# Performance work log

Measured on AMD Instinct MI355X. Metric: run time of the kernel, lower is better.

The kernel has to match this reference:

```python
import jax, jax.numpy as jnp
import numpy as np

T, D = 4096, 1024
S = 32768
DIST_DIM = 20
BINS = jnp.array([1, 2, 3, 4, 8, 16, 32, 64], dtype=jnp.int64)


def setup_inputs() -> dict:
    key = jax.random.key(0)
    ks = jax.random.split(key, 16)
    scale = 1.0 / np.sqrt(D)
    inp = {
        "embeds": jax.random.normal(ks[0], (T, D), dtype=jnp.float32),
        "states": jax.random.normal(ks[1], (T, D), dtype=jnp.float32),
        # MHA (1 head) projection params, torch Linear convention: x @ W.T + b
        "Wq": jax.random.normal(ks[2], (D, D), dtype=jnp.float32) * scale,
        "bq": jnp.zeros((D,), dtype=jnp.float32),
        "Wk": jax.random.normal(ks[3], (D, D), dtype=jnp.float32) * scale,
        "bk": jnp.zeros((D,), dtype=jnp.float32),
        "Wv": jax.random.normal(ks[4], (D, D), dtype=jnp.float32) * scale,
        "bv": jnp.zeros((D,), dtype=jnp.float32),
        "Wo": jax.random.normal(ks[5], (D, D), dtype=jnp.float32) * scale,
        "bo": jnp.zeros((D,), dtype=jnp.float32),
        # distance embedding table: len(bins)+1 = 9 rows
        "dist_embed": jax.random.normal(ks[6], (9, DIST_DIM), dtype=jnp.float32),
        "span_starts": jax.random.randint(ks[7], (S,), 0, T - 30, dtype=jnp.int64),
        "span_lengths": jax.random.randint(ks[8], (S,), 0, 30, dtype=jnp.int64),
    }
    return inp


def reference(embeds, states, Wq, bq, Wk, bk, Wv, bv, Wo, bo, dist_embed,
              span_starts, span_lengths):
    d = states.shape[1]
    # Single-head attention: query=states, key=states, value=embeds (seq len T, batch 1)
    q = states @ Wq.T + bq                      # [T, D]
    k = states @ Wk.T + bk                      # [T, D]
    v = embeds @ Wv.T + bv                      # [T, D]
    scores = (q @ k.T) / jnp.sqrt(jnp.asarray(d, q.dtype))   # [T, T]
    attn = jax.nn.softmax(scores, axis=-1)
    attn_embeds = (attn @ v) @ Wo.T + bo        # [T, D]

    ends = span_starts + span_lengths           # inclusive end, width 1..30
    # ragged per-span segment sum over [start, end] via prefix sums
    cs = jnp.concatenate([jnp.zeros((1, d), attn_embeds.dtype),
                          jnp.cumsum(attn_embeds, axis=0)], axis=0)  # [T+1, D]
    span_sum = cs[ends + 1] - cs[span_starts]   # [S, D]

    span_start_end = jnp.concatenate([states[span_starts], states[ends]], axis=1)  # [S, 2D]

    lengths = span_lengths + 1                  # len(span) = end - start + 1
    bin_idx = jnp.sum(lengths[:, None] > BINS[None, :], axis=-1)  # [S] in [0, 8]
    len_embed = dist_embed[bin_idx]             # [S, DIST_DIM] (dropout omitted: eval mode)

    return jnp.concatenate([span_sum, span_start_end, len_embed], axis=1)  # [S, 3D+20]
```

## Files before the change

### kernel.cpp

```cpp
#include <hip/hip_runtime.h>
#include <hip/hip_bf16.h>


typedef __attribute__((ext_vector_type(8))) short bf16x8;
typedef __attribute__((ext_vector_type(4))) short bf16x4;
typedef __attribute__((ext_vector_type(4))) float f32x4;

#define T_DIM 4096
#define D_DIM 1024
#define S_NUM 32768

#define GLOBAL_LOAD_LDS16(gptr, ldsptr)                                        \
  __builtin_amdgcn_global_load_lds(                                            \
      (const __attribute__((address_space(1))) void*)(gptr),                   \
      (__attribute__((address_space(3))) void*)(ldsptr), 16, 0, 0)

__global__ __launch_bounds__(256) void cast2_bf16(const float* __restrict__ a,
                                                  const float* __restrict__ b,
                                                  __hip_bfloat16* __restrict__ oa,
                                                  __hip_bfloat16* __restrict__ ob) {
  const float* s = blockIdx.z ? b : a;
  __hip_bfloat16* d = blockIdx.z ? ob : oa;
  int i = blockIdx.x * 256 + threadIdx.x;
  float2 v = ((const float2*)s)[i];
  __hip_bfloat162 o;
  o.x = __float2bfloat16(v.x);
  o.y = __float2bfloat16(v.y);
  ((__hip_bfloat162*)d)[i] = o;
}

__global__ __launch_bounds__(256) void cast3_bf16(const float* __restrict__ a,
                                                  const float* __restrict__ b,
                                                  const float* __restrict__ c,
                                                  __hip_bfloat16* __restrict__ oa,
                                                  __hip_bfloat16* __restrict__ ob,
                                                  __hip_bfloat16* __restrict__ oc) {
  const int z = blockIdx.z;
  const float* s = z == 0 ? a : z == 1 ? b : c;
  __hip_bfloat16* d = z == 0 ? oa : z == 1 ? ob : oc;
  int i = blockIdx.x * 256 + threadIdx.x;
  float2 v = ((const float2*)s)[i];
  __hip_bfloat162 o;
  o.x = __float2bfloat16(v.x);
  o.y = __float2bfloat16(v.y);
  ((__hip_bfloat162*)d)[i] = o;
}

__global__ __launch_bounds__(256) void transpose_cast_bf16(const float* __restrict__ in,
                                                           __hip_bfloat16* __restrict__ out) {
  __shared__ float tile[64][65];
  const int bx = blockIdx.x * 64;
  const int by = blockIdx.y * 64;
  const int t = threadIdx.x;
  const int r = t >> 4;
  const int c4 = (t & 15) * 4;
#pragma unroll
  for (int p = 0; p < 4; p++) {
    const float4 v = *(const float4*)&in[(size_t)(by + p * 16 + r) * D_DIM + bx + c4];
    tile[p * 16 + r][c4] = v.x;
    tile[p * 16 + r][c4 + 1] = v.y;
    tile[p * 16 + r][c4 + 2] = v.z;
    tile[p * 16 + r][c4 + 3] = v.w;
  }
  __syncthreads();
#pragma unroll
  for (int p = 0; p < 4; p++) {
    const int orow = p * 16 + r;
    bf16x4 o4;
#pragma unroll
    for (int q = 0; q < 4; q++) {
      __hip_bfloat16 h = __float2bfloat16(tile[c4 + q][orow]);
      o4[q] = *reinterpret_cast<short*>(&h);
    }
    *reinterpret_cast<bf16x4*>(&out[(size_t)(bx + orow) * D_DIM + by + c4]) = o4;
  }
}

__global__ __launch_bounds__(256) void zero_f32(float* __restrict__ p, int n) {
  int i = blockIdx.x * 256 + threadIdx.x;
  if (i < n) p[i] = 0.0f;
}

__global__ __launch_bounds__(256) void bias_fuse(const float* __restrict__ Wo,
                                                 const float* __restrict__ bv,
                                                 const float* __restrict__ bo,
                                                 float* __restrict__ bvo) {
  const int wave = threadIdx.x >> 6, lane = threadIdx.x & 63;
  const int row = blockIdx.x * 4 + wave;
  float s = 0.0f;
  for (int k = lane; k < D_DIM; k += 64) s += Wo[(size_t)row * D_DIM + k] * bv[k];
#pragma unroll
  for (int off = 32; off; off >>= 1) s += __shfl_xor(s, off);
  if (lane == 0) bvo[row] = s + bo[row];
}

__device__ __forceinline__ void gemm_core_128(const __hip_bfloat16* __restrict__ A,
                                              const __hip_bfloat16* __restrict__ B,
                                              int K, int bm, int bn,
                                              __hip_bfloat16* As,
                                              __hip_bfloat16* Bs,
                                              f32x4 acc[4][4]) {
  const int tid = threadIdx.x;
  const int wave = tid >> 6, lane = tid & 63;
  const int srow = lane >> 2, scol = (lane & 3) * 8;
  const __hip_bfloat16* Ag0 = A + (size_t)(bm + wave * 16 + srow) * K + scol;
  const __hip_bfloat16* Ag1 = Ag0 + (size_t)64 * K;
  const __hip_bfloat16* Bg0 = B + (size_t)(bn + wave * 16 + srow) * K + scol;
  const __hip_bfloat16* Bg1 = Bg0 + (size_t)64 * K;
  const int c0 = wave * 512, c1 = (4 + wave) * 512;
  const int wtr = (wave >> 1) * 64, wtc = (wave & 1) * 64;
  const int lr = lane & 15, lk = (lane >> 4) * 8;

  GLOBAL_LOAD_LDS16(Ag0, As + c0);
  GLOBAL_LOAD_LDS16(Ag1, As + c1);
  GLOBAL_LOAD_LDS16(Bg0, Bs + c0);
  GLOBAL_LOAD_LDS16(Bg1, Bs + c1);

  int cur = 0;
  for (int k0 = 0; k0 < K; k0 += 32) {
    __syncthreads();
    const int nxt = cur ^ 1;
    if (k0 + 32 < K) {
      const int kn = k0 + 32;
      GLOBAL_LOAD_LDS16(Ag0 + kn, As + nxt * 4096 + c0);
      GLOBAL_LOAD_LDS16(Ag1 + kn, As + nxt * 4096 + c1);
      GLOBAL_LOAD_LDS16(Bg0 + kn, Bs + nxt * 4096 + c0);
      GLOBAL_LOAD_LDS16(Bg1 + kn, Bs + nxt * 4096 + c1);
    }
    const __hip_bfloat16* a = As + cur * 4096;
    const __hip_bfloat16* b = Bs + cur * 4096;
    bf16x8 af[4], bfr[4];
#pragma unroll
    for (int i = 0; i < 4; i++)
      af[i] = *(const bf16x8*)&a[(wtr + i * 16 + lr) * 32 + lk];
#pragma unroll
    for (int j = 0; j < 4; j++)
      bfr[j] = *(const bf16x8*)&b[(wtc + j * 16 + lr) * 32 + lk];
#pragma unroll
    for (int i = 0; i < 4; i++)
#pragma unroll
      for (int j = 0; j < 4; j++)
        acc[i][j] = __builtin_amdgcn_mfma_f32_16x16x32_bf16(af[i], bfr[j], acc[i][j], 0, 0, 0);
    cur = nxt;
  }
}


__global__ __launch_bounds__(256) void wvo_gemm(const __hip_bfloat16* __restrict__ Wo_bf,
                                                const __hip_bfloat16* __restrict__ WvT_bf,
                                                __hip_bfloat16* __restrict__ Wvo_bf) {
  __shared__ __hip_bfloat16 As[2 * 128 * 32];
  __shared__ __hip_bfloat16 Bs[2 * 128 * 32];
  const int bm = blockIdx.y * 128, bn = blockIdx.x * 128;
  const int wave = threadIdx.x >> 6, lane = threadIdx.x & 63;
  const int wtr = (wave >> 1) * 64, wtc = (wave & 1) * 64;
  const int lr = lane & 15;
  f32x4 acc[4][4] = {};
  gemm_core_128(Wo_bf, WvT_bf, D_DIM, bm, bn, As, Bs, acc);
#pragma unroll
  for (int j = 0; j < 4; j++) {
    const int col = bn + wtc + j * 16 + lr;
#pragma unroll
    for (int i = 0; i < 4; i++)
#pragma unroll
      for (int r = 0; r < 4; r++) {
        const int row = bm + wtr + i * 16 + (lane >> 4) * 4 + r;
        Wvo_bf[(size_t)row * D_DIM + col] = __float2bfloat16(acc[i][j][r]);
      }
  }
}

__global__ __launch_bounds__(256) void qkv_gemm(const __hip_bfloat16* __restrict__ states_bf,
                                                const __hip_bfloat16* __restrict__ embeds_bf,
                                                const __hip_bfloat16* __restrict__ Wq,
                                                const __hip_bfloat16* __restrict__ Wk,
                                                const __hip_bfloat16* __restrict__ Wvo,
                                                const float* __restrict__ bq,
                                                const float* __restrict__ bk,
                                                __hip_bfloat16* __restrict__ q,
                                                __hip_bfloat16* __restrict__ k,
                                                __hip_bfloat16* __restrict__ vT) {
  __shared__ __hip_bfloat16 As[2 * 128 * 32];
  __shared__ __hip_bfloat16 Bs[2 * 128 * 32];
  const int z = blockIdx.z;
  const __hip_bfloat16* A = (z == 2) ? embeds_bf : states_bf;
  const __hip_bfloat16* B = (z == 0) ? Wq : (z == 1) ? Wk : Wvo;
  const float* bias = (z == 0) ? bq : bk;
  const int bm = blockIdx.y * 128, bn = blockIdx.x * 128;
  const int wave = threadIdx.x >> 6, lane = threadIdx.x & 63;
  const int wtr = (wave >> 1) * 64, wtc = (wave & 1) * 64;
  const int lr = lane & 15;
  f32x4 acc[4][4] = {};
  gemm_core_128(A, B, D_DIM, bm, bn, As, Bs, acc);

#pragma unroll
  for (int j = 0; j < 4; j++) {
    const int col = bn + wtc + j * 16 + lr;
    const float bb = (z == 2) ? 0.0f : bias[col];
#pragma unroll
    for (int i = 0; i < 4; i++) {
#pragma unroll
      for (int r = 0; r < 4; r++) {
        const int row = bm + wtr + i * 16 + (lane >> 4) * 4 + r;
        const __hip_bfloat16 val = __float2bfloat16(acc[i][j][r] + bb);
        if (z == 0)
          q[(size_t)row * D_DIM + col] = val;
        else if (z == 1)
          k[(size_t)row * D_DIM + col] = val;
        else
          vT[(size_t)col * T_DIM + row] = val;
      }
    }
  }
}

__global__ __launch_bounds__(256) void scoresP_gemm(const __hip_bfloat16* __restrict__ q,
                                                    const __hip_bfloat16* __restrict__ k,
                                                    __hip_bfloat16* __restrict__ P,
                                                    float* __restrict__ l) {
  __shared__ __hip_bfloat16 As[2 * 128 * 32];
  __shared__ __hip_bfloat16 Bs[2 * 128 * 32];
  const int bm = blockIdx.y * 128, bn = blockIdx.x * 128;
  const int wave = threadIdx.x >> 6, lane = threadIdx.x & 63;
  const int wtr = (wave >> 1) * 64, wtc = (wave & 1) * 64;
  const int lr = lane & 15;
  f32x4 acc[4][4] = {};
  gemm_core_128(q, k, D_DIM, bm, bn, As, Bs, acc);

  float rowsum[4][4];
#pragma unroll
  for (int i = 0; i < 4; i++)
#pragma unroll
    for (int r = 0; r < 4; r++) rowsum[i][r] = 0.0f;

#pragma unroll
  for (int j = 0; j < 4; j++) {
    const int col = bn + wtc + j * 16 + lr;
#pragma unroll
    for (int i = 0; i < 4; i++) {
#pragma unroll
      for (int r = 0; r < 4; r++) {
        const int row = bm + wtr + i * 16 + (lane >> 4) * 4 + r;
        const float e = __expf(acc[i][j][r] * 0.03125f);
        P[(size_t)row * T_DIM + col] = __float2bfloat16(e);
        rowsum[i][r] += e;
      }
    }
  }
#pragma unroll
  for (int off = 1; off < 16; off <<= 1)
#pragma unroll
    for (int i = 0; i < 4; i++)
#pragma unroll
      for (int r = 0; r < 4; r++)
        rowsum[i][r] += __shfl_xor(rowsum[i][r], off);
  if ((lane & 15) == 0) {
#pragma unroll
    for (int i = 0; i < 4; i++)
#pragma unroll
      for (int r = 0; r < 4; r++) {
        const int row = bm + wtr + i * 16 + (lane >> 4) * 4 + r;
        atomicAdd(&l[row], rowsum[i][r]);
      }
  }
}

__global__ __launch_bounds__(256) void pv_gemm(const __hip_bfloat16* __restrict__ P,
                                               const __hip_bfloat16* __restrict__ vT,
                                               const float* __restrict__ l,
                                               const float* __restrict__ bvo,
                                               float* __restrict__ ao) {
  __shared__ __hip_bfloat16 As[2 * 128 * 32];
  __shared__ __hip_bfloat16 Bs[2 * 128 * 32];
  const int bm = blockIdx.y * 128, bn = blockIdx.x * 128;
  const int wave = threadIdx.x >> 6, lane = threadIdx.x & 63;
  const int wtr = (wave >> 1) * 64, wtc = (wave & 1) * 64;
  const int lr = lane & 15;
  f32x4 acc[4][4] = {};
  gemm_core_128(P, vT, T_DIM, bm, bn, As, Bs, acc);

  float inv[4][4];
#pragma unroll
  for (int i = 0; i < 4; i++)
#pragma unroll
    for (int r = 0; r < 4; r++) {
      const int row = bm + wtr + i * 16 + (lane >> 4) * 4 + r;
      inv[i][r] = 1.0f / l[row];
    }
#pragma unroll
  for (int j = 0; j < 4; j++) {
    const int col = bn + wtc + j * 16 + lr;
    const float bb = bvo[col];
#pragma unroll
    for (int i = 0; i < 4; i++)
#pragma unroll
      for (int r = 0; r < 4; r++) {
        const int row = bm + wtr + i * 16 + (lane >> 4) * 4 + r;
        ao[(size_t)row * D_DIM + col] = acc[i][j][r] * inv[i][r] + bb;
      }
  }
}

__global__ __launch_bounds__(256) void colsum_chunks(const float* __restrict__ x,
                                                     float* __restrict__ part) {
  const int col = blockIdx.x * 256 + threadIdx.x;
  const int ch = blockIdx.y;
  const float* p = x + (size_t)ch * 64 * D_DIM + col;
  float s = 0.0f;
#pragma unroll 8
  for (int i = 0; i < 64; i++) s += p[i * D_DIM];
  part[ch * D_DIM + col] = s;
}

__global__ __launch_bounds__(256) void scan_chunks(float* part) {
  const int col = blockIdx.x * 256 + threadIdx.x;
  float run = 0.0f;
  for (int ch = 0; ch < 64; ch++) {
    const float t = part[ch * D_DIM + col];
    part[ch * D_DIM + col] = run;
    run += t;
  }
}

__global__ __launch_bounds__(256) void write_cs(const float* __restrict__ x,
                                                const float* __restrict__ part,
                                                float* __restrict__ cs) {
  const int col = blockIdx.x * 256 + threadIdx.x;
  const int ch = blockIdx.y;
  float run = part[ch * D_DIM + col];
  if (ch == 0) cs[col] = 0.0f;
  const float* p = x + (size_t)ch * 64 * D_DIM + col;
  float* q = cs + ((size_t)(ch * 64 + 1)) * D_DIM + col;
  for (int i = 0; i < 64; i++) {
    run += p[i * D_DIM];
    q[i * D_DIM] = run;
  }
}

__global__ __launch_bounds__(256) void span_gather(const float* __restrict__ cs,
                                                   const float* __restrict__ states,
                                                   const float* __restrict__ dist,
                                                   const int* __restrict__ starts,
                                                   const int* __restrict__ lens,
                                                   float* __restrict__ out) {
  const int s = blockIdx.x;
  const int start = starts[s];
  const int len = lens[s];
  const int end = start + len;
  const int length = len + 1;
  const int bin = (length > 1) + (length > 2) + (length > 3) + (length > 4) +
                  (length > 8) + (length > 16) + (length > 32) + (length > 64);
  const f32x4* csS = (const f32x4*)(cs + (size_t)start * D_DIM);
  const f32x4* csE = (const f32x4*)(cs + (size_t)(end + 1) * D_DIM);
  const f32x4* stS = (const f32x4*)(states + (size_t)start * D_DIM);
  const f32x4* stE = (const f32x4*)(states + (size_t)end * D_DIM);
  const f32x4* de = (const f32x4*)(dist + bin * 20);
  f32x4* o = (f32x4*)(out + (size_t)s * 3092);
  for (int j = threadIdx.x; j < 773; j += 256) {
    f32x4 r;
    if (j < 256) {
      r = csE[j] - csS[j];
    } else if (j < 512) {
      r = stS[j - 256];
    } else if (j < 768) {
      r = stE[j - 512];
    } else {
      r = de[j - 768];
    }
    __builtin_nontemporal_store(r, o + j);
  }
}

extern "C" void kernel_launch(void* const* d_in, const int* in_sizes, int n_in,
                              void* d_out, int out_size, void* d_ws, size_t ws_size,
                              hipStream_t stream) {
  const float* embeds = (const float*)d_in[0];
  const float* states = (const float*)d_in[1];
  const float* Wq = (const float*)d_in[2];
  const float* bq = (const float*)d_in[3];
  const float* Wk = (const float*)d_in[4];
  const float* bk = (const float*)d_in[5];
  const float* Wv = (const float*)d_in[6];
  const float* bv = (const float*)d_in[7];
  const float* Wo = (const float*)d_in[8];
  const float* bo = (const float*)d_in[9];
  const float* dist = (const float*)d_in[10];
  const int* starts = (const int*)d_in[11];
  const int* lens = (const int*)d_in[12];
  float* out = (float*)d_out;

  const size_t TD = (size_t)T_DIM * D_DIM;
  const size_t DD = (size_t)D_DIM * D_DIM;
  const size_t TT = (size_t)T_DIM * T_DIM;

  char* w = (char*)d_ws;
  size_t off = 0;
  auto alloc = [&](size_t bytes) {
    char* p = w + off;
    off = (off + bytes + 255) & ~(size_t)255;
    return p;
  };
  __hip_bfloat16* states_bf = (__hip_bfloat16*)alloc(TD * 2);
  __hip_bfloat16* embeds_bf = (__hip_bfloat16*)alloc(TD * 2);
  __hip_bfloat16* Wq_bf = (__hip_bfloat16*)alloc(DD * 2);
  __hip_bfloat16* Wk_bf = (__hip_bfloat16*)alloc(DD * 2);
  __hip_bfloat16* Wo_bf = (__hip_bfloat16*)alloc(DD * 2);
  __hip_bfloat16* WvT_bf = (__hip_bfloat16*)alloc(DD * 2);
  __hip_bfloat16* Wvo_bf = (__hip_bfloat16*)alloc(DD * 2);
  __hip_bfloat16* q_bf = (__hip_bfloat16*)alloc(TD * 2);
  __hip_bfloat16* k_bf = (__hip_bfloat16*)alloc(TD * 2);
  __hip_bfloat16* vT_bf = (__hip_bfloat16*)alloc(TD * 2);
  __hip_bfloat16* P_bf = (__hip_bfloat16*)alloc(TT * 2);
  float* l_sum = (float*)alloc(T_DIM * 4);
  float* bvo = (float*)alloc(D_DIM * 4);
  float* ao = (float*)alloc(TD * 4);
  float* cs = (float*)alloc((size_t)(T_DIM + 1) * D_DIM * 4);
  float* part = (float*)alloc(64 * D_DIM * 4);
  if (off > ws_size) return;

  cast2_bf16<<<dim3(TD / 512, 1, 2), 256, 0, stream>>>(states, embeds, states_bf, embeds_bf);
  cast3_bf16<<<dim3(DD / 512, 1, 3), 256, 0, stream>>>(Wq, Wk, Wo, Wq_bf, Wk_bf, Wo_bf);
  transpose_cast_bf16<<<dim3(16, 16), 256, 0, stream>>>(Wv, WvT_bf);
  zero_f32<<<T_DIM / 256, 256, 0, stream>>>(l_sum, T_DIM);
  bias_fuse<<<D_DIM / 4, 256, 0, stream>>>(Wo, bv, bo, bvo);

  wvo_gemm<<<dim3(D_DIM / 128, D_DIM / 128), 256, 0, stream>>>(Wo_bf, WvT_bf, Wvo_bf);

  qkv_gemm<<<dim3(D_DIM / 128, T_DIM / 128, 3), 256, 0, stream>>>(
      states_bf, embeds_bf, Wq_bf, Wk_bf, Wvo_bf, bq, bk, q_bf, k_bf, vT_bf);

  scoresP_gemm<<<dim3(T_DIM / 128, T_DIM / 128), 256, 0, stream>>>(q_bf, k_bf, P_bf, l_sum);

  pv_gemm<<<dim3(D_DIM / 128, T_DIM / 128), 256, 0, stream>>>(P_bf, vT_bf, l_sum, bvo, ao);

  colsum_chunks<<<dim3(4, 64), 256, 0, stream>>>(ao, part);
  scan_chunks<<<4, 256, 0, stream>>>(part);
  write_cs<<<dim3(4, 64), 256, 0, stream>>>(ao, part, cs);

  span_gather<<<S_NUM, 256, 0, stream>>>(cs, states, dist, starts, lens, out);
}
```

Measured before the change: 737.7 us.

## Split-K the Wvo and PV GEMMs and sort spans by start for gather locality

The Wvo GEMM is split four ways and the PV GEMM two ways along K. Each split writes fp32 partials, and separate combine kernels reduce them, applying normalization and bias for PV. This raises the number of blocks on a GPU with many CUs, since the PV grid was only 256 blocks. Separately, spans are bucketed by start index through a histogram, scan and scatter, so span_gather visits neighbouring rows of cs and states consecutively for better cache reuse. The cost is extra kernel launches, fp32 partial-buffer traffic and atomics. The zero kernel is widened to clear the histogram, which relies on hist being allocated right after l_sum.

```diff
diff --git a/kernel.cpp b/kernel.cpp
--- a/kernel.cpp
+++ b/kernel.cpp
@@ -96,17 +96,18 @@
 
 __device__ __forceinline__ void gemm_core_128(const __hip_bfloat16* __restrict__ A,
                                               const __hip_bfloat16* __restrict__ B,
-                                              int K, int bm, int bn,
+                                              int K, int lda, int ldb,
+                                              int bm, int bn,
                                               __hip_bfloat16* As,
                                               __hip_bfloat16* Bs,
                                               f32x4 acc[4][4]) {
   const int tid = threadIdx.x;
   const int wave = tid >> 6, lane = tid & 63;
   const int srow = lane >> 2, scol = (lane & 3) * 8;
-  const __hip_bfloat16* Ag0 = A + (size_t)(bm + wave * 16 + srow) * K + scol;
-  const __hip_bfloat16* Ag1 = Ag0 + (size_t)64 * K;
-  const __hip_bfloat16* Bg0 = B + (size_t)(bn + wave * 16 + srow) * K + scol;
-  const __hip_bfloat16* Bg1 = Bg0 + (size_t)64 * K;
+  const __hip_bfloat16* Ag0 = A + (size_t)(bm + wave * 16 + srow) * lda + scol;
+  const __hip_bfloat16* Ag1 = Ag0 + (size_t)64 * lda;
+  const __hip_bfloat16* Bg0 = B + (size_t)(bn + wave * 16 + srow) * ldb + scol;
+  const __hip_bfloat16* Bg1 = Bg0 + (size_t)64 * ldb;
   const int c0 = wave * 512, c1 = (4 + wave) * 512;
   const int wtr = (wave >> 1) * 64, wtc = (wave & 1) * 64;
   const int lr = lane & 15, lk = (lane >> 4) * 8;
@@ -146,17 +147,19 @@
 }
 
 
-__global__ __launch_bounds__(256) void wvo_gemm(const __hip_bfloat16* __restrict__ Wo_bf,
-                                                const __hip_bfloat16* __restrict__ WvT_bf,
-                                                __hip_bfloat16* __restrict__ Wvo_bf) {
+__global__ __launch_bounds__(256) void wvo_gemm_splitk(const __hip_bfloat16* __restrict__ Wo_bf,
+                                                       const __hip_bfloat16* __restrict__ WvT_bf,
+                                                       float* __restrict__ part) {
   __shared__ __hip_bfloat16 As[2 * 128 * 32];
   __shared__ __hip_bfloat16 Bs[2 * 128 * 32];
+  const int z = blockIdx.z;
   const int bm = blockIdx.y * 128, bn = blockIdx.x * 128;
   const int wave = threadIdx.x >> 6, lane = threadIdx.x & 63;
   const int wtr = (wave >> 1) * 64, wtc = (wave & 1) * 64;
   const int lr = lane & 15;
   f32x4 acc[4][4] = {};
-  gemm_core_128(Wo_bf, WvT_bf, D_DIM, bm, bn, As, Bs, acc);
+  gemm_core_128(Wo_bf + z * 256, WvT_bf + z * 256, 256, D_DIM, D_DIM, bm, bn, As, Bs, acc);
+  float* dst = part + (size_t)z * D_DIM * D_DIM;
 #pragma unroll
   for (int j = 0; j < 4; j++) {
     const int col = bn + wtc + j * 16 + lr;
@@ -165,9 +168,26 @@
 #pragma unroll
       for (int r = 0; r < 4; r++) {
         const int row = bm + wtr + i * 16 + (lane >> 4) * 4 + r;
-        Wvo_bf[(size_t)row * D_DIM + col] = __float2bfloat16(acc[i][j][r]);
+        dst[(size_t)row * D_DIM + col] = acc[i][j][r];
       }
   }
+}
+
+__global__ __launch_bounds__(256) void wvo_combine(const float* __restrict__ part,
+                                                   __hip_bfloat16* __restrict__ out) {
+  const size_t idx = (size_t)blockIdx.x * 256 + threadIdx.x;
+  const size_t n = (size_t)D_DIM * D_DIM / 4;
+  f32x4 s = ((const f32x4*)part)[idx];
+  s += ((const f32x4*)part)[idx + n];
+  s += ((const f32x4*)part)[idx + 2 * n];
+  s += ((const f32x4*)part)[idx + 3 * n];
+  bf16x4 o;
+#pragma unroll
+  for (int q = 0; q < 4; q++) {
+    __hip_bfloat16 h = __float2bfloat16(s[q]);
+    o[q] = *reinterpret_cast<short*>(&h);
+  }
+  ((bf16x4*)out)[idx] = o;
 }
 
 __global__ __launch_bounds__(256) void qkv_gemm(const __hip_bfloat16* __restrict__ states_bf,
@@ -191,7 +211,7 @@
   const int wtr = (wave >> 1) * 64, wtc = (wave & 1) * 64;
   const int lr = lane & 15;
   f32x4 acc[4][4] = {};
-  gemm_core_128(A, B, D_DIM, bm, bn, As, Bs, acc);
+  gemm_core_128(A, B, D_DIM, D_DIM, D_DIM, bm, bn, As, Bs, acc);
 
 #pragma unroll
   for (int j = 0; j < 4; j++) {
@@ -225,7 +245,7 @@
   const int wtr = (wave >> 1) * 64, wtc = (wave & 1) * 64;
   const int lr = lane & 15;
   f32x4 acc[4][4] = {};
-  gemm_core_128(q, k, D_DIM, bm, bn, As, Bs, acc);
+  gemm_core_128(q, k, D_DIM, D_DIM, D_DIM, bm, bn, As, Bs, acc);
 
   float rowsum[4][4];
 #pragma unroll
@@ -265,40 +285,46 @@
   }
 }
 
-__global__ __launch_bounds__(256) void pv_gemm(const __hip_bfloat16* __restrict__ P,
-                                               const __hip_bfloat16* __restrict__ vT,
-                                               const float* __restrict__ l,
-                                               const float* __restrict__ bvo,
-                                               float* __restrict__ ao) {
+__global__ __launch_bounds__(256) void pv_gemm_splitk(const __hip_bfloat16* __restrict__ P,
+                                                      const __hip_bfloat16* __restrict__ vT,
+                                                      float* __restrict__ part) {
   __shared__ __hip_bfloat16 As[2 * 128 * 32];
   __shared__ __hip_bfloat16 Bs[2 * 128 * 32];
+  const int z = blockIdx.z;
   const int bm = blockIdx.y * 128, bn = blockIdx.x * 128;
   const int wave = threadIdx.x >> 6, lane = threadIdx.x & 63;
   const int wtr = (wave >> 1) * 64, wtc = (wave & 1) * 64;
   const int lr = lane & 15;
   f32x4 acc[4][4] = {};
-  gemm_core_128(P, vT, T_DIM, bm, bn, As, Bs, acc);
-
-  float inv[4][4];
-#pragma unroll
-  for (int i = 0; i < 4; i++)
-#pragma unroll
-    for (int r = 0; r < 4; r++) {
-      const int row = bm + wtr + i * 16 + (lane >> 4) * 4 + r;
-      inv[i][r] = 1.0f / l[row];
-    }
+  gemm_core_128(P + z * 2048, vT + z * 2048, 2048, T_DIM, T_DIM, bm, bn, As, Bs, acc);
+  float* dst = part + (size_t)z * T_DIM * D_DIM;
 #pragma unroll
   for (int j = 0; j < 4; j++) {
     const int col = bn + wtc + j * 16 + lr;
-    const float bb = bvo[col];
 #pragma unroll
     for (int i = 0; i < 4; i++)
 #pragma unroll
       for (int r = 0; r < 4; r++) {
         const int row = bm + wtr + i * 16 + (lane >> 4) * 4 + r;
-        ao[(size_t)row * D_DIM + col] = acc[i][j][r] * inv[i][r] + bb;
+        dst[(size_t)row * D_DIM + col] = acc[i][j][r];
       }
   }
+}
+
+__global__ __launch_bounds__(256) void pv_combine(const float* __restrict__ part,
+                                                  const float* __restrict__ l,
+                                                  const float* __restrict__ bvo,
+                                                  float* __restrict__ ao) {
+  const size_t idx = (size_t)blockIdx.x * 256 + threadIdx.x;
+  const size_t n = (size_t)T_DIM * D_DIM / 4;
+  const int row = (int)(idx >> 8);
+  const int c4 = (int)(idx & 255) * 4;
+  const float inv = 1.0f / l[row];
+  f32x4 a = ((const f32x4*)part)[idx];
+  f32x4 b = ((const f32x4*)part)[idx + n];
+  f32x4 bb = *(const f32x4*)(bvo + c4);
+  f32x4 r = (a + b) * inv + bb;
+  ((f32x4*)ao)[idx] = r;
 }
 
 __global__ __launch_bounds__(256) void colsum_chunks(const float* __restrict__ x,
@@ -337,13 +363,50 @@
   }
 }
 
+__global__ __launch_bounds__(256) void hist_k(const int* __restrict__ starts,
+                                              int* __restrict__ hist) {
+  const int s = blockIdx.x * 256 + threadIdx.x;
+  atomicAdd(&hist[starts[s]], 1);
+}
+
+__global__ __launch_bounds__(1024) void scan_hist(const int* __restrict__ hist,
+                                                  int* __restrict__ offs) {
+  __shared__ int sums[1024];
+  const int t = threadIdx.x;
+  const int v0 = hist[t * 4], v1 = hist[t * 4 + 1];
+  const int v2 = hist[t * 4 + 2], v3 = hist[t * 4 + 3];
+  const int tot = v0 + v1 + v2 + v3;
+  sums[t] = tot;
+  __syncthreads();
+  for (int off = 1; off < 1024; off <<= 1) {
+    const int x = (t >= off) ? sums[t - off] : 0;
+    __syncthreads();
+    sums[t] += x;
+    __syncthreads();
+  }
+  const int excl = sums[t] - tot;
+  offs[t * 4] = excl;
+  offs[t * 4 + 1] = excl + v0;
+  offs[t * 4 + 2] = excl + v0 + v1;
+  offs[t * 4 + 3] = excl + v0 + v1 + v2;
+}
+
+__global__ __launch_bounds__(256) void scatter_k(const int* __restrict__ starts,
+                                                 int* __restrict__ offs,
+                                                 int* __restrict__ perm) {
+  const int s = blockIdx.x * 256 + threadIdx.x;
+  const int pos = atomicAdd(&offs[starts[s]], 1);
+  perm[pos] = s;
+}
+
 __global__ __launch_bounds__(256) void span_gather(const float* __restrict__ cs,
                                                    const float* __restrict__ states,
                                                    const float* __restrict__ dist,
                                                    const int* __restrict__ starts,
                                                    const int* __restrict__ lens,
+                                                   const int* __restrict__ perm,
                                                    float* __restrict__ out) {
-  const int s = blockIdx.x;
+  const int s = perm[blockIdx.x];
   const int start = starts[s];
   const int len = lens[s];
   const int end = start + len;
@@ -412,30 +475,41 @@
   __hip_bfloat16* vT_bf = (__hip_bfloat16*)alloc(TD * 2);
   __hip_bfloat16* P_bf = (__hip_bfloat16*)alloc(TT * 2);
   float* l_sum = (float*)alloc(T_DIM * 4);
+  int* hist = (int*)alloc(T_DIM * 4);
+  int* offs = (int*)alloc(T_DIM * 4);
+  int* perm = (int*)alloc(S_NUM * 4);
   float* bvo = (float*)alloc(D_DIM * 4);
   float* ao = (float*)alloc(TD * 4);
   float* cs = (float*)alloc((size_t)(T_DIM + 1) * D_DIM * 4);
   float* part = (float*)alloc(64 * D_DIM * 4);
+  float* wvo_part = (float*)alloc(4 * DD * 4);
+  float* pv_part = (float*)alloc(2 * TD * 4);
   if (off > ws_size) return;
 
   cast2_bf16<<<dim3(TD / 512, 1, 2), 256, 0, stream>>>(states, embeds, states_bf, embeds_bf);
   cast3_bf16<<<dim3(DD / 512, 1, 3), 256, 0, stream>>>(Wq, Wk, Wo, Wq_bf, Wk_bf, Wo_bf);
   transpose_cast_bf16<<<dim3(16, 16), 256, 0, stream>>>(Wv, WvT_bf);
-  zero_f32<<<T_DIM / 256, 256, 0, stream>>>(l_sum, T_DIM);
+  zero_f32<<<2 * T_DIM / 256, 256, 0, stream>>>(l_sum, 2 * T_DIM);
   bias_fuse<<<D_DIM / 4, 256, 0, stream>>>(Wo, bv, bo, bvo);
 
-  wvo_gemm<<<dim3(D_DIM / 128, D_DIM / 128), 256, 0, stream>>>(Wo_bf, WvT_bf, Wvo_bf);
+  hist_k<<<S_NUM / 256, 256, 0, stream>>>(starts, hist);
+  scan_hist<<<1, 1024, 0, stream>>>(hist, offs);
+  scatter_k<<<S_NUM / 256, 256, 0, stream>>>(starts, offs, perm);
+
+  wvo_gemm_splitk<<<dim3(D_DIM / 128, D_DIM / 128, 4), 256, 0, stream>>>(Wo_bf, WvT_bf, wvo_part);
+  wvo_combine<<<DD / 1024, 256, 0, stream>>>(wvo_part, Wvo_bf);
 
   qkv_gemm<<<dim3(D_DIM / 128, T_DIM / 128, 3), 256, 0, stream>>>(
       states_bf, embeds_bf, Wq_bf, Wk_bf, Wvo_bf, bq, bk, q_bf, k_bf, vT_bf);
 
   scoresP_gemm<<<dim3(T_DIM / 128, T_DIM / 128), 256, 0, stream>>>(q_bf, k_bf, P_bf, l_sum);
 
-  pv_gemm<<<dim3(D_DIM / 128, T_DIM / 128), 256, 0, stream>>>(P_bf, vT_bf, l_sum, bvo, ao);
+  pv_gemm_splitk<<<dim3(D_DIM / 128, T_DIM / 128, 2), 256, 0, stream>>>(P_bf, vT_bf, pv_part);
+  pv_combine<<<TD / 1024, 256, 0, stream>>>(pv_part, l_sum, bvo, ao);
 
   colsum_chunks<<<dim3(4, 64), 256, 0, stream>>>(ao, part);
   scan_chunks<<<4, 256, 0, stream>>>(part);
   write_cs<<<dim3(4, 64), 256, 0, stream>>>(ao, part, cs);
 
-  span_gather<<<S_NUM, 256, 0, stream>>>(cs, states, dist, starts, lens, out);
-}
+  span_gather<<<S_NUM, 256, 0, stream>>>(cs, states, dist, starts, lens, perm, out);
+}
```

Measured after the change: 712.0 us. 3.5% less time.
